# Kernel optimization log

Measured on AMD Instinct MI355X. Metric: run time of the kernel, lower is better.

The kernel has to match this reference:

```python
import jax, jax.numpy as jnp
import numpy as np

ACT_DIM = 768
DICT_SIZE = 32768
S0 = 4096          # top-level latent size (dict_size // prod(lower sizes))
S1 = 8             # lower_level_latent_sizes[0]
K = 64             # per-token top-k (applied globally as k * batch)


def setup_inputs() -> dict:
    key = jax.random.key(0)
    ks = jax.random.split(key, 7)
    scale_e = 1.0 / np.sqrt(ACT_DIM)
    scale_d = 1.0 / np.sqrt(DICT_SIZE)
    return {
        "x": jax.random.normal(ks[0], (4096, ACT_DIM), dtype=jnp.float32),
        "W0": jax.random.normal(ks[1], (S0, ACT_DIM), dtype=jnp.float32) * scale_e,
        "b0": jnp.zeros((S0,), dtype=jnp.float32),
        "W1": jax.random.normal(ks[2], (DICT_SIZE, ACT_DIM), dtype=jnp.float32) * scale_e,
        "b1": jnp.zeros((DICT_SIZE,), dtype=jnp.float32),
        "Wd": jax.random.normal(ks[3], (ACT_DIM, DICT_SIZE), dtype=jnp.float32) * scale_d,
        "b_dec": jnp.zeros((ACT_DIM,), dtype=jnp.float32),
    }


def reference(x, W0, b0, W1, b1, Wd, b_dec):
    B = x.shape[0]
    x_centered = x - b_dec                                   # [B, D]
    # hierarchical relu encoders
    l0 = jax.nn.relu(x_centered @ W0.T + b0)                 # [B, S0]
    l1 = jax.nn.relu(x_centered @ W1.T + b1)                 # [B, S0*S1]
    # multiplicative gating: lower-level gate broadcast over finest level
    final_dense = (l1.reshape(B, S0, S1) * l0[:, :, None]).reshape(B, S0 * S1)
    # global batch top-k over flattened [B * dict_size]
    flat = final_dense.reshape(-1)
    k_for_batch = min(K * B, flat.shape[0])
    vals, idx = jax.lax.top_k(flat, k_for_batch)
    sparse_flat = jnp.zeros_like(flat).at[idx].set(vals)
    encoded = sparse_flat.reshape(B, S0 * S1)
    # decode
    x_hat = encoded @ Wd.T + b_dec                           # [B, D]
    return x_hat
```

## Files before the change

kernel.cpp:

```cpp
#include <hip/hip_runtime.h>
#include <stdint.h>

#define DDIM 768
#define BROWS 4096
#define S0N 4096
#define DICT 32768
#define KTOT 262144u
#define PREF 2.0f
#define DELTA 4e-3f
#define CAND_CAP 8388608u
#define BAND_CAP 4096

static constexpr size_t OFF_XH   = 0;
static constexpr size_t OFF_XL   = 6291456;
static constexpr size_t OFF_W0H  = 12582912;
static constexpr size_t OFF_W0L  = 18874368;
static constexpr size_t OFF_W1H  = 25165824;
static constexpr size_t OFF_W1L  = 75497472;
static constexpr size_t OFF_WDT  = 0;
static constexpr size_t OFF_L0   = 125829120;
static constexpr size_t OFF_CTRL = 192937984;
static constexpr size_t OFF_ROWC = 193069056;
static constexpr size_t OFF_ROWD = 193085440;
static constexpr size_t OFF_CAND = 201474048;
static constexpr size_t WS_NEED  = 268582912;


typedef __attribute__((ext_vector_type(8))) short bf16x8;
typedef __attribute__((ext_vector_type(4))) float f32x4;

__device__ __forceinline__ unsigned umin_(unsigned a, unsigned b) { return a < b ? a : b; }
__device__ __forceinline__ float relu_(float v) { return v > 0.f ? v : 0.f; }

__device__ __forceinline__ unsigned short f2bf(float f) {
    union { float f; unsigned u; } v; v.f = f;
    unsigned r = v.u + 0x7FFFu + ((v.u >> 16) & 1u);
    return (unsigned short)(r >> 16);
}
__device__ __forceinline__ float bf2f(unsigned short h) {
    union { float f; unsigned u; } v; v.u = ((unsigned)h) << 16;
    return v.f;
}
__device__ __forceinline__ void split1(float a, short& h, short& l) {
    unsigned short hb = f2bf(a);
    float rem = a - bf2f(hb);
    h = (short)hb;
    l = (short)f2bf(rem);
}

__device__ __forceinline__ void gl16(const void* g, void* l) {
    __builtin_amdgcn_global_load_lds(
        (const __attribute__((address_space(1))) void*)g,
        (__attribute__((address_space(3))) void*)l,
        16, 0, 0);
}

__global__ void k_split_x(const float* __restrict__ x, const float* __restrict__ b_dec,
                          short* __restrict__ XH, short* __restrict__ XL) {
    int i = blockIdx.x * 256 + threadIdx.x;
    float4 xv = ((const float4*)x)[i];
    int d = (i % (DDIM / 4)) * 4;
    float4 bv = *(const float4*)(b_dec + d);
    float a[4] = {xv.x - bv.x, xv.y - bv.y, xv.z - bv.z, xv.w - bv.w};
    short4 h, lo;
    split1(a[0], h.x, lo.x); split1(a[1], h.y, lo.y);
    split1(a[2], h.z, lo.z); split1(a[3], h.w, lo.w);
    ((short4*)XH)[i] = h;
    ((short4*)XL)[i] = lo;
}

__global__ void k_split_w(const float* __restrict__ W, short* __restrict__ H,
                          short* __restrict__ L) {
    int i = blockIdx.x * 256 + threadIdx.x;
    float4 wv = ((const float4*)W)[i];
    short4 h, lo;
    split1(wv.x, h.x, lo.x); split1(wv.y, h.y, lo.y);
    split1(wv.z, h.z, lo.z); split1(wv.w, h.w, lo.w);
    ((short4*)H)[i] = h;
    ((short4*)L)[i] = lo;
}

__global__ void k_transpose(const float* __restrict__ Wd, float* __restrict__ WdT) {
    __shared__ float tile[32][33];
    int j0 = blockIdx.x * 32, d0 = blockIdx.y * 32;
    int tx = threadIdx.x & 31, ty = threadIdx.x >> 5;
#pragma unroll
    for (int i = 0; i < 4; ++i)
        tile[ty + i * 8][tx] = Wd[(size_t)(d0 + ty + i * 8) * DICT + j0 + tx];
    __syncthreads();
#pragma unroll
    for (int i = 0; i < 4; ++i)
        WdT[(size_t)(j0 + ty + i * 8) * DDIM + d0 + tx] = tile[tx][ty + i * 8];
}

template<int EPI>
__launch_bounds__(512, 2) __global__
void k_mm(const short* __restrict__ XH, const short* __restrict__ XL,
          const short* __restrict__ WH, const short* __restrict__ WL,
          const float* __restrict__ bias, float* __restrict__ l0buf,
          uint2* __restrict__ cand, unsigned* __restrict__ ctrl) {
    __shared__ __align__(16) char smem[131072];

    const int t = threadIdx.x;
    const int w = t >> 6, l = t & 63;
    const int wm = w >> 2, wn = w & 3;
    const int lr = l & 15, lk = l >> 4;

    const int nwg = gridDim.x;
    const int bid = blockIdx.x;
    const int swz = (bid & 7) * (nwg >> 3) + (bid >> 3);
    const int bm = (swz & 15) << 8;
    const int bn = (swz >> 4) << 8;

    unsigned idxA[4], idxB[4];
#pragma unroll
    for (int q = 0; q < 4; ++q) {
        const int ab = w * 4 + q;
        idxA[q] = (unsigned)(bm + (ab >> 4) * 128 + ((ab >> 1) & 7) * 16 + lr) * 768u
                + (unsigned)((ab & 1) * 32 + lk * 8);
        idxB[q] = (unsigned)(bn + (ab >> 3) * 64 + ((ab >> 1) & 3) * 16 + lr) * 768u
                + (unsigned)((ab & 1) * 32 + lk * 8);
    }

    f32x4 acc[8][4];
#pragma unroll
    for (int i = 0; i < 8; ++i)
#pragma unroll
        for (int j = 0; j < 4; ++j) acc[i][j] = (f32x4){0.f, 0.f, 0.f, 0.f};

#pragma unroll
    for (int q = 0; q < 4; ++q) {
        gl16(XH + idxA[q], smem + (w * 4 + q) * 1024);
        gl16(WH + idxB[q], smem + 65536 + (w * 4 + q) * 1024);
    }
    asm volatile("s_waitcnt vmcnt(0)" ::: "memory");
    __syncthreads();

    int cur = 0;
    for (int kt = 0; kt < 36; ++kt) {
        const int ktn = kt + 1;
        const bool hn = ktn < 36;
        const short* An; const short* Bn; unsigned kbn;
        if (ktn < 12)      { An = XH; Bn = WH; kbn = (unsigned)ktn * 64u; }
        else if (ktn < 24) { An = XH; Bn = WL; kbn = (unsigned)(ktn - 12) * 64u; }
        else               { An = XL; Bn = WH; kbn = (unsigned)(ktn - 24) * 64u; }
        char* stA = smem + (cur ^ 1) * 32768;
        char* stB = smem + 65536 + (cur ^ 1) * 32768;
        const short* rA = (const short*)(smem + cur * 32768);
        const short* rB = (const short*)(smem + 65536 + cur * 32768);

        bf16x8 bf[4];
#pragma unroll
        for (int p = 0; p < 4; ++p) {
            const int ks = p >> 1, mh = p & 1;
            bf16x8 af[4];
#pragma unroll
            for (int m2 = 0; m2 < 4; ++m2) {
                const int mi = mh * 4 + m2;
                af[m2] = *(const bf16x8*)(rA + ((wm * 16 + mi * 2 + ks) * 1024 + l * 16) / 2);
            }
            if (mh == 0) {
#pragma unroll
                for (int nj = 0; nj < 4; ++nj)
                    bf[nj] = *(const bf16x8*)(rB + ((wn * 8 + nj * 2 + ks) * 1024 + l * 16) / 2);
            }
            if (hn) {
                gl16(An + idxA[p] + kbn, stA + (w * 4 + p) * 1024);
                gl16(Bn + idxB[p] + kbn, stB + (w * 4 + p) * 1024);
            }
            __builtin_amdgcn_s_barrier();
            asm volatile("s_waitcnt lgkmcnt(0)" ::: "memory");
            __builtin_amdgcn_sched_barrier(0);
            __builtin_amdgcn_s_setprio(1);
#pragma unroll
            for (int m2 = 0; m2 < 4; ++m2)
#pragma unroll
                for (int nj = 0; nj < 4; ++nj)
                    acc[mh * 4 + m2][nj] = __builtin_amdgcn_mfma_f32_16x16x32_bf16(
                        af[m2], bf[nj], acc[mh * 4 + m2][nj], 0, 0, 0);
            __builtin_amdgcn_s_setprio(0);
            __builtin_amdgcn_s_barrier();
        }
        asm volatile("s_waitcnt vmcnt(0)" ::: "memory");
        __builtin_amdgcn_s_barrier();
        cur ^= 1;
    }
    __syncthreads();

    if constexpr (EPI == 0) {
#pragma unroll
        for (int mi = 0; mi < 8; ++mi) {
#pragma unroll
            for (int r = 0; r < 4; ++r) {
                const int row = bm + wm * 128 + mi * 16 + lk * 4 + r;
                float* orow = l0buf + (size_t)row * S0N;
#pragma unroll
                for (int nj = 0; nj < 4; ++nj) {
                    const int col = bn + wn * 64 + nj * 16 + lr;
                    orow[col] = relu_(acc[mi][nj][r] + bias[col]);
                }
            }
        }
    } else {
        unsigned* pscan = (unsigned*)smem;
        unsigned cnt = 0;
#pragma unroll
        for (int mi = 0; mi < 8; ++mi)
#pragma unroll
            for (int nj = 0; nj < 4; ++nj)
#pragma unroll
                for (int r = 0; r < 4; ++r) {
                    const int row = bm + wm * 128 + mi * 16 + lk * 4 + r;
                    const int col = bn + wn * 64 + nj * 16 + lr;
                    float v = relu_(acc[mi][nj][r] + bias[col]);
                    v *= l0buf[(size_t)row * S0N + (col >> 3)];
                    acc[mi][nj][r] = v;
                    cnt += (v >= PREF) ? 1u : 0u;
                }
        pscan[t] = cnt;
        __syncthreads();
        for (int s = 1; s < 512; s <<= 1) {
            unsigned v2 = (t >= s) ? pscan[t - s] : 0u;
            __syncthreads();
            pscan[t] += v2;
            __syncthreads();
        }
        if (t == 511) pscan[512] = atomicAdd(&ctrl[0], pscan[511]);
        __syncthreads();
        unsigned off = pscan[512] + pscan[t] - cnt;
#pragma unroll
        for (int mi = 0; mi < 8; ++mi)
#pragma unroll
            for (int nj = 0; nj < 4; ++nj)
#pragma unroll
                for (int r = 0; r < 4; ++r) {
                    const float v = acc[mi][nj][r];
                    if (v >= PREF) {
                        const int row = bm + wm * 128 + mi * 16 + lk * 4 + r;
                        const int col = bn + wn * 64 + nj * 16 + lr;
                        if (off < CAND_CAP)
                            cand[off] = make_uint2(__float_as_uint(v),
                                                   ((unsigned)row << 15) | (unsigned)col);
                        ++off;
                    }
                }
    }
}

__global__ void k_hist1(const uint2* __restrict__ cand, unsigned* __restrict__ ctrl) {
    __shared__ unsigned h[2048];
    for (int i = threadIdx.x; i < 2048; i += 256) h[i] = 0;
    __syncthreads();
    unsigned n = umin_(ctrl[0], CAND_CAP);
    for (unsigned i = blockIdx.x * 256 + threadIdx.x; i < n; i += gridDim.x * 256)
        atomicAdd(&h[cand[i].x >> 20], 1u);
    __syncthreads();
    unsigned* hist = ctrl + 256;
    for (int i = threadIdx.x; i < 2048; i += 256)
        if (h[i]) atomicAdd(&hist[i], h[i]);
}

__global__ void k_scan1(unsigned* __restrict__ ctrl) {
    __shared__ unsigned hs[2048];
    __shared__ unsigned cs[256];
    const unsigned* h = ctrl + 256;
    int t = threadIdx.x;
    for (int i = t; i < 2048; i += 256) hs[i] = h[i];
    __syncthreads();
    unsigned s = 0;
    for (int b = 0; b < 8; ++b) s += hs[t * 8 + b];
    cs[t] = s;
    __syncthreads();
    if (t == 0) {
        unsigned cum = 0, T = 0, cb = 0;
        for (int c = 255; c >= 0; --c) {
            if (cum + cs[c] >= KTOT) {
                for (int b = c * 8 + 7; b >= c * 8; --b) {
                    cum += hs[b];
                    if (cum >= KTOT) { T = (unsigned)b; cb = cum - hs[b]; break; }
                }
                break;
            }
            cum += cs[c];
        }
        ctrl[1] = T; ctrl[2] = cb;
    }
}

__global__ void k_hist2(const uint2* __restrict__ cand, unsigned* __restrict__ ctrl) {
    unsigned n = umin_(ctrl[0], CAND_CAP);
    unsigned T = ctrl[1];
    unsigned* hist2 = ctrl + 2304;
    for (unsigned i = blockIdx.x * 256 + threadIdx.x; i < n; i += gridDim.x * 256) {
        unsigned u = cand[i].x;
        if ((u >> 20) == T) atomicAdd(&hist2[(u >> 8) & 0xFFFu], 1u);
    }
}

__global__ void k_scan2(unsigned* __restrict__ ctrl) {
    __shared__ unsigned hs[4096];
    __shared__ unsigned cs[256];
    const unsigned* h = ctrl + 2304;
    int t = threadIdx.x;
    for (int i = t; i < 4096; i += 256) hs[i] = h[i];
    __syncthreads();
    unsigned s = 0;
    for (int b = 0; b < 16; ++b) s += hs[t * 16 + b];
    cs[t] = s;
    __syncthreads();
    if (t == 0) {
        unsigned cum = ctrl[2], T2 = 0;
        for (int c = 255; c >= 0; --c) {
            if (cum + cs[c] >= KTOT) {
                for (int b = c * 16 + 15; b >= c * 16; --b) {
                    cum += hs[b];
                    if (cum >= KTOT) { T2 = (unsigned)b; break; }
                }
                break;
            }
            cum += cs[c];
        }
        ctrl[3] = (ctrl[1] << 12) | T2;
    }
}

__global__ void k_band(const uint2* __restrict__ cand, unsigned* __restrict__ ctrl) {
    __shared__ unsigned lhi;
    if (threadIdx.x == 0) lhi = 0;
    __syncthreads();
    unsigned n = umin_(ctrl[0], CAND_CAP);
    unsigned H = ctrl[3];
    float lo = __uint_as_float(H << 8) - DELTA;
    float hi = __uint_as_float((H + 1u) << 8) + DELTA;
    unsigned* band_idx = ctrl + 6400;
    unsigned my = 0;
    for (unsigned i = blockIdx.x * 256 + threadIdx.x; i < n; i += gridDim.x * 256) {
        float v = __uint_as_float(cand[i].x);
        if (v > hi) ++my;
        else if (v >= lo) {
            unsigned p = atomicAdd(&ctrl[5], 1u);
            if (p < BAND_CAP) band_idx[p] = cand[i].y;
        }
    }
    atomicAdd(&lhi, my);
    __syncthreads();
    if (threadIdx.x == 0 && lhi) atomicAdd(&ctrl[4], lhi);
}

__global__ void k_f64(const float* __restrict__ x, const float* __restrict__ b_dec,
                      const float* __restrict__ W0, const float* __restrict__ b0,
                      const float* __restrict__ W1, const float* __restrict__ b1,
                      const unsigned* __restrict__ ctrl, double* __restrict__ band_v) {
    unsigned n = umin_(ctrl[5], BAND_CAP);
    unsigned bi = blockIdx.x;
    if (bi >= n) return;
    const unsigned* band_idx = ctrl + 6400;
    unsigned idx = band_idx[bi];
    int b = idx >> 15, j = idx & 32767, s0 = j >> 3;
    int lane = threadIdx.x;
    const float* xr = x + (size_t)b * DDIM;
    const float* w1 = W1 + (size_t)j * DDIM;
    const float* w0 = W0 + (size_t)s0 * DDIM;
    double d1 = 0.0, d0 = 0.0;
    for (int k = lane; k < DDIM; k += 64) {
        double xv = (double)xr[k] - (double)b_dec[k];
        d1 += xv * (double)w1[k];
        d0 += xv * (double)w0[k];
    }
    for (int off = 32; off; off >>= 1) {
        d1 += __shfl_down(d1, off);
        d0 += __shfl_down(d0, off);
    }
    if (lane == 0) {
        double l1v = d1 + (double)b1[j];  l1v = l1v > 0.0 ? l1v : 0.0;
        double l0v = d0 + (double)b0[s0]; l0v = l0v > 0.0 ? l0v : 0.0;
        band_v[bi] = l1v * l0v;
    }
}

__global__ void k_final(unsigned* __restrict__ ctrl, const double* __restrict__ band_v,
                        uint2* __restrict__ extra) {
    __shared__ unsigned long long skey[BAND_CAP];
    __shared__ unsigned sidx[BAND_CAP];
    int t = threadIdx.x;
    unsigned n = umin_(ctrl[5], BAND_CAP);
    const unsigned* band_idx = ctrl + 6400;
    for (int i = t; i < BAND_CAP; i += 256) {
        if ((unsigned)i < n) {
            skey[i] = (unsigned long long)__double_as_longlong(band_v[i]);
            sidx[i] = band_idx[i];
        } else {
            skey[i] = 0ull; sidx[i] = 0xFFFFFFFFu;
        }
    }
    __syncthreads();
    for (int kk = 2; kk <= BAND_CAP; kk <<= 1) {
        for (int jj = kk >> 1; jj > 0; jj >>= 1) {
            for (int i = t; i < BAND_CAP; i += 256) {
                int ixj = i ^ jj;
                if (ixj > i) {
                    unsigned long long ka = skey[i], kb = skey[ixj];
                    unsigned ia = sidx[i], ib = sidx[ixj];
                    bool ab = (ka > kb) || (ka == kb && ia < ib);
                    bool asc = ((i & kk) == 0);
                    if (asc ? !ab : ab) {
                        skey[i] = kb; skey[ixj] = ka;
                        sidx[i] = ib; sidx[ixj] = ia;
                    }
                }
            }
            __syncthreads();
        }
    }
    unsigned c_hi = ctrl[4];
    unsigned k_rem = (c_hi < KTOT) ? (KTOT - c_hi) : 0u;
    if (k_rem > n) k_rem = n;
    if (t == 0) ctrl[6] = k_rem;
    for (unsigned i = t; i < k_rem; i += 256)
        extra[i] = make_uint2(sidx[i],
                              __float_as_uint((float)__longlong_as_double((long long)skey[i])));
}

__global__ void k_rows_a(const uint2* __restrict__ cand, const unsigned* __restrict__ ctrl,
                         unsigned* __restrict__ rowc, uint2* __restrict__ rowd) {
    unsigned n = umin_(ctrl[0], CAND_CAP);
    unsigned H = ctrl[3];
    float hi = __uint_as_float((H + 1u) << 8) + DELTA;
    for (unsigned i = blockIdx.x * 256 + threadIdx.x; i < n; i += gridDim.x * 256) {
        unsigned u = cand[i].x;
        if (__uint_as_float(u) > hi) {
            unsigned idx = cand[i].y;
            unsigned b = idx >> 15;
            unsigned p = atomicAdd(&rowc[b], 1u);
            if (p < 256u) rowd[(b << 8) + p] = make_uint2(idx & 32767u, u);
        }
    }
}

__global__ void k_rows_b(const unsigned* __restrict__ ctrl, const uint2* __restrict__ extra,
                         unsigned* __restrict__ rowc, uint2* __restrict__ rowd) {
    unsigned k_rem = ctrl[6];
    for (unsigned i = blockIdx.x * 256 + threadIdx.x; i < k_rem; i += gridDim.x * 256) {
        unsigned idx = extra[i].x;
        unsigned b = idx >> 15;
        unsigned p = atomicAdd(&rowc[b], 1u);
        if (p < 256u) rowd[(b << 8) + p] = make_uint2(idx & 32767u, extra[i].y);
    }
}

__launch_bounds__(256) __global__
void k_decode(const uint2* __restrict__ rowd, const unsigned* __restrict__ rowc,
              const float* __restrict__ WdT, const float* __restrict__ b_dec,
              float* __restrict__ out) {
    __shared__ uint2 e[256];
    int b = blockIdx.x, t = threadIdx.x;
    unsigned c = rowc[b]; if (c > 256u) c = 256u;
    if ((unsigned)t < c) e[t] = rowd[(b << 8) + t];
    __syncthreads();
    float a0 = b_dec[t], a1 = b_dec[t + 256], a2 = b_dec[t + 512];
#pragma unroll 4
    for (unsigned i = 0; i < c; ++i) {
        float v = __uint_as_float(e[i].y);
        const float* w = WdT + (size_t)e[i].x * DDIM;
        a0 = fmaf(v, w[t], a0);
        a1 = fmaf(v, w[t + 256], a1);
        a2 = fmaf(v, w[t + 512], a2);
    }
    float* o = out + (size_t)b * DDIM;
    o[t] = a0; o[t + 256] = a1; o[t + 512] = a2;
}

extern "C" void kernel_launch(void* const* d_in, const int* in_sizes, int n_in,
                              void* d_out, int out_size, void* d_ws, size_t ws_size,
                              hipStream_t stream) {
    const float* x     = (const float*)d_in[0];
    const float* W0    = (const float*)d_in[1];
    const float* b0    = (const float*)d_in[2];
    const float* W1    = (const float*)d_in[3];
    const float* b1    = (const float*)d_in[4];
    const float* Wd    = (const float*)d_in[5];
    const float* b_dec = (const float*)d_in[6];
    float* out = (float*)d_out;

    if (ws_size < WS_NEED) {
        hipMemsetAsync(d_out, 0, (size_t)out_size * sizeof(float), stream);
        return;
    }

    char* ws = (char*)d_ws;
    short*    XH     = (short*)(ws + OFF_XH);
    short*    XL     = (short*)(ws + OFF_XL);
    short*    W0H    = (short*)(ws + OFF_W0H);
    short*    W0L    = (short*)(ws + OFF_W0L);
    short*    W1H    = (short*)(ws + OFF_W1H);
    short*    W1L    = (short*)(ws + OFF_W1L);
    float*    WdT    = (float*)(ws + OFF_WDT);
    float*    l0     = (float*)(ws + OFF_L0);
    unsigned* ctrl   = (unsigned*)(ws + OFF_CTRL);
    double*   band_v = (double*)(ws + OFF_CTRL + 65536);
    uint2*    extra  = (uint2*)(ws + OFF_CTRL + 98304);
    unsigned* rowc   = (unsigned*)(ws + OFF_ROWC);
    uint2*    rowd   = (uint2*)(ws + OFF_ROWD);
    uint2*    cand   = (uint2*)(ws + OFF_CAND);

    hipMemsetAsync(ctrl, 0, 6400 * sizeof(unsigned), stream);
    hipMemsetAsync(rowc, 0, BROWS * sizeof(unsigned), stream);

    k_split_x<<<(BROWS * DDIM / 4) / 256, 256, 0, stream>>>(x, b_dec, XH, XL);
    k_split_w<<<(S0N * DDIM / 4) / 256, 256, 0, stream>>>(W0, W0H, W0L);
    k_split_w<<<(DICT * DDIM / 4) / 256, 256, 0, stream>>>(W1, W1H, W1L);

    k_mm<0><<<(S0N / 256) * 16, 512, 0, stream>>>(XH, XL, W0H, W0L, b0, l0, nullptr, nullptr);
    k_mm<1><<<(DICT / 256) * 16, 512, 0, stream>>>(XH, XL, W1H, W1L, b1, l0, cand, ctrl);

    k_transpose<<<dim3(DICT / 32, DDIM / 32), 256, 0, stream>>>(Wd, WdT);

    k_hist1<<<1024, 256, 0, stream>>>(cand, ctrl);
    k_scan1<<<1, 256, 0, stream>>>(ctrl);
    k_hist2<<<1024, 256, 0, stream>>>(cand, ctrl);
    k_scan2<<<1, 256, 0, stream>>>(ctrl);
    k_band<<<1024, 256, 0, stream>>>(cand, ctrl);
    k_f64<<<BAND_CAP, 64, 0, stream>>>(x, b_dec, W0, b0, W1, b1, ctrl, band_v);
    k_final<<<1, 256, 0, stream>>>(ctrl, band_v, extra);

    k_rows_a<<<1024, 256, 0, stream>>>(cand, ctrl, rowc, rowd);
    k_rows_b<<<32, 256, 0, stream>>>(ctrl, extra, rowc, rowd);
    k_decode<<<BROWS, 256, 0, stream>>>(rowd, rowc, WdT, b_dec, out);
}
```

Before: 1.310 ms.

## Restructure GEMM mainloop to issue next-tile loads up front and drop per-phase barriers

The double-buffered GEMM main loop now issues all global-to-LDS loads for the next K tile at the start of each iteration. It waits with a partial vmcnt so only the current tile's loads must finish, then runs all 64 MFMAs per iteration without the per-phase barriers and lgkmcnt waits. This cuts synchronisation overhead and gives the compiler freedom to interleave LDS reads with MFMAs. The partial vmcnt(8) wait depends on exactly 8 outstanding loads per wave, and the barriers must still protect buffer reuse.

```diff
diff --git a/kernel.cpp b/kernel.cpp
--- a/kernel.cpp
+++ b/kernel.cpp
@@ -133,57 +133,48 @@
         gl16(XH + idxA[q], smem + (w * 4 + q) * 1024);
         gl16(WH + idxB[q], smem + 65536 + (w * 4 + q) * 1024);
     }
-    asm volatile("s_waitcnt vmcnt(0)" ::: "memory");
-    __syncthreads();
-
-    int cur = 0;
+
     for (int kt = 0; kt < 36; ++kt) {
+        const int cur = kt & 1;
+        __builtin_amdgcn_s_barrier();
         const int ktn = kt + 1;
-        const bool hn = ktn < 36;
-        const short* An; const short* Bn; unsigned kbn;
-        if (ktn < 12)      { An = XH; Bn = WH; kbn = (unsigned)ktn * 64u; }
-        else if (ktn < 24) { An = XH; Bn = WL; kbn = (unsigned)(ktn - 12) * 64u; }
-        else               { An = XL; Bn = WH; kbn = (unsigned)(ktn - 24) * 64u; }
-        char* stA = smem + (cur ^ 1) * 32768;
-        char* stB = smem + 65536 + (cur ^ 1) * 32768;
+        if (ktn < 36) {
+            const short* An; const short* Bn; unsigned kbn;
+            if (ktn < 12)      { An = XH; Bn = WH; kbn = (unsigned)ktn * 64u; }
+            else if (ktn < 24) { An = XH; Bn = WL; kbn = (unsigned)(ktn - 12) * 64u; }
+            else               { An = XL; Bn = WH; kbn = (unsigned)(ktn - 24) * 64u; }
+            char* stA = smem + (cur ^ 1) * 32768;
+            char* stB = smem + 65536 + (cur ^ 1) * 32768;
+#pragma unroll
+            for (int q = 0; q < 4; ++q) {
+                gl16(An + idxA[q] + kbn, stA + (w * 4 + q) * 1024);
+                gl16(Bn + idxB[q] + kbn, stB + (w * 4 + q) * 1024);
+            }
+            asm volatile("s_waitcnt vmcnt(8)" ::: "memory");
+        } else {
+            asm volatile("s_waitcnt vmcnt(0)" ::: "memory");
+        }
+        __builtin_amdgcn_s_barrier();
+
         const short* rA = (const short*)(smem + cur * 32768);
         const short* rB = (const short*)(smem + 65536 + cur * 32768);
-
-        bf16x8 bf[4];
-#pragma unroll
-        for (int p = 0; p < 4; ++p) {
-            const int ks = p >> 1, mh = p & 1;
-            bf16x8 af[4];
-#pragma unroll
-            for (int m2 = 0; m2 < 4; ++m2) {
-                const int mi = mh * 4 + m2;
-                af[m2] = *(const bf16x8*)(rA + ((wm * 16 + mi * 2 + ks) * 1024 + l * 16) / 2);
+        __builtin_amdgcn_s_setprio(1);
+#pragma unroll
+        for (int ks = 0; ks < 2; ++ks) {
+            bf16x8 bfr[4];
+#pragma unroll
+            for (int nj = 0; nj < 4; ++nj)
+                bfr[nj] = *(const bf16x8*)(rB + ((wn * 8 + nj * 2 + ks) * 1024 + l * 16) / 2);
+#pragma unroll
+            for (int mi = 0; mi < 8; ++mi) {
+                bf16x8 af = *(const bf16x8*)(rA + ((wm * 16 + mi * 2 + ks) * 1024 + l * 16) / 2);
+#pragma unroll
+                for (int nj = 0; nj < 4; ++nj)
+                    acc[mi][nj] = __builtin_amdgcn_mfma_f32_16x16x32_bf16(
+                        af, bfr[nj], acc[mi][nj], 0, 0, 0);
             }
-            if (mh == 0) {
-#pragma unroll
-                for (int nj = 0; nj < 4; ++nj)
-                    bf[nj] = *(const bf16x8*)(rB + ((wn * 8 + nj * 2 + ks) * 1024 + l * 16) / 2);
-            }
-            if (hn) {
-                gl16(An + idxA[p] + kbn, stA + (w * 4 + p) * 1024);
-                gl16(Bn + idxB[p] + kbn, stB + (w * 4 + p) * 1024);
-            }
-            __builtin_amdgcn_s_barrier();
-            asm volatile("s_waitcnt lgkmcnt(0)" ::: "memory");
-            __builtin_amdgcn_sched_barrier(0);
-            __builtin_amdgcn_s_setprio(1);
-#pragma unroll
-            for (int m2 = 0; m2 < 4; ++m2)
-#pragma unroll
-                for (int nj = 0; nj < 4; ++nj)
-                    acc[mh * 4 + m2][nj] = __builtin_amdgcn_mfma_f32_16x16x32_bf16(
-                        af[m2], bf[nj], acc[mh * 4 + m2][nj], 0, 0, 0);
-            __builtin_amdgcn_s_setprio(0);
-            __builtin_amdgcn_s_barrier();
-        }
-        asm volatile("s_waitcnt vmcnt(0)" ::: "memory");
-        __builtin_amdgcn_s_barrier();
-        cur ^= 1;
+        }
+        __builtin_amdgcn_s_setprio(0);
     }
     __syncthreads();
 
```

Result: slower. 1.368 ms (+4.4%).
